# Kernel optimization log

Measured on AMD Instinct MI355X. Metric: run time of the kernel, lower is better.

The kernel has to match this reference:

```python
import jax, jax.numpy as jnp
import numpy as np

DIM = 192
HEADS = 6
HEAD_DIM = DIM // HEADS
WH, WW = 8, 8
N = WH * WW
SCALE = HEAD_DIM ** -0.5


def relative_position_index(wh, ww):
    ch, cw = np.meshgrid(np.arange(wh), np.arange(ww), indexing='ij')
    coords = np.stack([ch.ravel(), cw.ravel()])            # [2, N]
    rel = coords[:, :, None] - coords[:, None, :]          # [2, N, N]
    rel = rel.transpose(1, 2, 0)
    rel[:, :, 0] += wh - 1
    rel[:, :, 1] += ww - 1
    rel[:, :, 0] *= 2 * ww - 1
    return jnp.asarray(rel.sum(-1))                        # [N, N] int


REL_IDX = relative_position_index(WH, WW)


def setup_inputs() -> dict:
    key = jax.random.key(0)
    ks = jax.random.split(key, 12)
    B_ = 4096
    nW = 64
    s = DIM ** -0.5
    inp = {
        'lr_up_windows': jax.random.normal(ks[0], (B_, N, DIM), jnp.float32),
        'ref_down_up_windows': jax.random.normal(ks[1], (B_, N, DIM), jnp.float32),
        'ref_windows': jax.random.normal(ks[2], (B_, N, DIM), jnp.float32),
        'mask': jnp.zeros((nW, N, N), jnp.float32),
        'Wq': jax.random.normal(ks[3], (DIM, DIM), jnp.float32) * s,
        'bq': jnp.zeros((DIM,), jnp.float32),
        'Wk': jax.random.normal(ks[4], (DIM, DIM), jnp.float32) * s,
        'bk': jnp.zeros((DIM,), jnp.float32),
        'Wv': jax.random.normal(ks[5], (DIM, DIM), jnp.float32) * s,
        'bv': jnp.zeros((DIM,), jnp.float32),
        'Wp': jax.random.normal(ks[6], (DIM, DIM), jnp.float32) * s,
        'bp': jnp.zeros((DIM,), jnp.float32),
        'bias_table': jax.random.normal(ks[7], ((2 * WH - 1) * (2 * WW - 1), HEADS), jnp.float32) * 0.02,
    }
    return inp


def reference(lr_up_windows, ref_down_up_windows, ref_windows, mask,
              Wq, bq, Wk, bk, Wv, bv, Wp, bp, bias_table):
    B_, n, C = lr_up_windows.shape
    # projections ([in, out] weights; x @ W + b)
    q = (lr_up_windows @ Wq + bq).reshape(B_, n, HEADS, HEAD_DIM).transpose(0, 2, 1, 3)
    k = (ref_down_up_windows @ Wk + bk).reshape(B_, n, HEADS, HEAD_DIM).transpose(0, 2, 1, 3)
    v = (ref_windows @ Wv + bv).reshape(B_, n, HEADS, HEAD_DIM).transpose(0, 2, 1, 3)
    attn = jnp.einsum('bhnd,bhmd->bhnm', q * SCALE, k)     # [B_, H, N, N]
    rpb = bias_table[REL_IDX]                               # [N, N, H]
    attn = attn + rpb.transpose(2, 0, 1)[None]
    nW = mask.shape[0]
    attn = attn.reshape(B_ // nW, nW, HEADS, n, n) + mask[None, :, None]
    attn = attn.reshape(B_, HEADS, n, n)
    attn = jax.nn.softmax(attn, axis=-1)
    x = jnp.einsum('bhnm,bhmd->bhnd', attn, v).transpose(0, 2, 1, 3).reshape(B_, n, C)
    return x @ Wp + bp
```

## Files before the change

### kernel.cpp

```cpp
#include <hip/hip_runtime.h>
#include <hip/hip_bf16.h>
#include <stdint.h>

typedef short s16x8 __attribute__((ext_vector_type(8)));
typedef short s16x4 __attribute__((ext_vector_type(4)));
typedef float f32x4 __attribute__((ext_vector_type(4)));

#define MFMA16(a, b, c) __builtin_amdgcn_mfma_f32_16x16x32_bf16((a), (b), (c), 0, 0, 0)

__device__ __forceinline__ unsigned short f2bf(float f) {
  union { float f; uint32_t u; } x; x.f = f;
  uint32_t u = x.u;
  return (unsigned short)((u + 0x7FFFu + ((u >> 16) & 1u)) >> 16);
}
__device__ __forceinline__ float bf2f(unsigned short h) {
  union { uint32_t u; float f; } x; x.u = ((uint32_t)h) << 16;
  return x.f;
}
__device__ __forceinline__ void glds16(const void* g, void* l) {
  __builtin_amdgcn_global_load_lds((const __attribute__((address_space(1))) void*)g,
                                   (__attribute__((address_space(3))) void*)l, 16, 0, 0);
}

__global__ __launch_bounds__(256) void prep_weights(
    const float* __restrict__ Wq, const float* __restrict__ Wk,
    const float* __restrict__ Wv, const float* __restrict__ Wp,
    unsigned short* __restrict__ wt) {
  int idx = blockIdx.x * 256 + threadIdx.x;
  if (idx >= 4 * 36864) return;
  int mat = idx / 36864, rem = idx % 36864;
  int n = rem / 192, k = rem % 192;
  const float* W = (mat == 0) ? Wq : (mat == 1) ? Wk : (mat == 2) ? Wv : Wp;
  wt[idx] = f2bf(W[k * 192 + n]);
}

__global__ __launch_bounds__(256) void prep_rpb(
    const float* __restrict__ bias_table, unsigned short* __restrict__ rpb) {
  int idx = blockIdx.x * 256 + threadIdx.x;
  if (idx >= 6 * 4096) return;
  int h = idx / 4096, r = idx % 4096;
  int i = r >> 6, j = r & 63;
  int dh = (i >> 3) - (j >> 3) + 7;
  int dw = (i & 7) - (j & 7) + 7;
  rpb[idx] = f2bf(bias_table[(dh * 15 + dw) * 6 + h]);
}

__global__ __launch_bounds__(256, 3) void pass1_proj(
    const float* __restrict__ X1g, const float* __restrict__ X2g,
    const float* __restrict__ X3g,
    const float* __restrict__ bq, const float* __restrict__ bk,
    const float* __restrict__ bv,
    const unsigned short* __restrict__ wt,
    char* __restrict__ qkv, int B_) {
  extern __shared__ char p1lds[];
  unsigned short* xs = (unsigned short*)p1lds;
  char* ob = p1lds + 25600;
  const int which = blockIdx.x / B_;
  const int w = blockIdx.x - which * B_;
  const int tid = threadIdx.x;
  const int lane = tid & 63;
  const int wv = tid >> 6;
  const int l16 = lane & 15, lq = lane >> 4;
  const float* Xb =
      ((which == 0) ? X1g : (which == 1) ? X2g : X3g) + (size_t)w * 12288;
  const unsigned short* W = wt + which * 36864;
  const int nt0 = wv * 3;

  const float4* Xb4 = (const float4*)Xb;
  float4 xr[12];
#pragma unroll
  for (int r = 0; r < 6; ++r) {
    int p = r * 256 + tid;
    xr[2 * r]     = Xb4[2 * p];
    xr[2 * r + 1] = Xb4[2 * p + 1];
  }

  s16x8 wf[3][6];
#pragma unroll
  for (int t = 0; t < 3; ++t) {
    const unsigned short* wc = W + (size_t)((nt0 + t) * 16 + l16) * 192 + lq * 8;
#pragma unroll
    for (int ks = 0; ks < 6; ++ks) wf[t][ks] = *(const s16x8*)(wc + ks * 32);
  }
  f32x4 bqk[3];
  float bvv[3];
  if (which < 2) {
    const float* bias = which ? bk : bq;
#pragma unroll
    for (int t = 0; t < 3; ++t)
      bqk[t] = *(const f32x4*)&bias[(nt0 + t) * 16 + lq * 4];
  } else {
#pragma unroll
    for (int t = 0; t < 3; ++t) bvv[t] = bv[(nt0 + t) * 16 + l16];
  }

#pragma unroll
  for (int r = 0; r < 6; ++r) {
    int p = r * 256 + tid;
    int row = p / 24, k8 = p - row * 24;
    const float4& a = xr[2 * r];
    const float4& c = xr[2 * r + 1];
    s16x8 t;
    t[0] = (short)f2bf(a.x); t[1] = (short)f2bf(a.y);
    t[2] = (short)f2bf(a.z); t[3] = (short)f2bf(a.w);
    t[4] = (short)f2bf(c.x); t[5] = (short)f2bf(c.y);
    t[6] = (short)f2bf(c.z); t[7] = (short)f2bf(c.w);
    *(s16x8*)&xs[row * 200 + k8 * 8] = t;
  }
  __syncthreads();

  const float scale = (which == 0) ? 0.17677669529663689f : 1.0f;

#pragma unroll
  for (int mi = 0; mi < 4; ++mi) {
    s16x8 xf[6];
    const unsigned short* pr = xs + (mi * 16 + l16) * 200 + lq * 8;
#pragma unroll
    for (int ks = 0; ks < 6; ++ks) xf[ks] = *(const s16x8*)(pr + ks * 32);
    if (which < 2) {
      int tok = mi * 16 + l16;
#pragma unroll
      for (int t = 0; t < 3; ++t) {
        f32x4 acc = bqk[t];
#pragma unroll
        for (int ks = 0; ks < 6; ++ks) acc = MFMA16(wf[t][ks], xf[ks], acc);
        s16x4 pv;
#pragma unroll
        for (int q = 0; q < 4; ++q) pv[q] = (short)f2bf(acc[q] * scale);
        int c = (nt0 + t) * 2 + (lq >> 1);
        *(s16x4*)(ob + tok * 384 + ((c ^ (tok & 7)) << 4) + (lq & 1) * 8) = pv;
      }
    } else {
#pragma unroll
      for (int t = 0; t < 3; ++t) {
        f32x4 acc = {bvv[t], bvv[t], bvv[t], bvv[t]};
#pragma unroll
        for (int ks = 0; ks < 6; ++ks) acc = MFMA16(xf[ks], wf[t][ks], acc);
        int d = (nt0 + t) * 16 + l16;
        int c = (mi >> 1) * 4 + lq;
        s16x4 pv;
#pragma unroll
        for (int q = 0; q < 4; ++q) pv[q] = (short)f2bf(acc[q]);
        *(s16x4*)(ob + d * 128 + ((c ^ (d & 7)) << 4) + (mi & 1) * 8) = pv;
      }
    }
  }
  __syncthreads();

  char* gdst = qkv + (size_t)w * 73728 + which * 24576;
#pragma unroll
  for (int r = 0; r < 6; ++r) {
    int i = (r * 256 + tid) * 16;
    *(float4*)(gdst + i) = *(const float4*)(ob + i);
  }
}

__global__ __launch_bounds__(512, 4) void pass2_attn(
    const char* __restrict__ qkv, const float* __restrict__ maskg,
    const unsigned short* __restrict__ rpb, const float* __restrict__ bp,
    const unsigned short* __restrict__ wt, float* __restrict__ out, int nW) {
  extern __shared__ char lds[];
  const int b = blockIdx.x, tid = threadIdx.x;
  const int wv = tid >> 6, lane = tid & 63;
  const int l16 = lane & 15, lq = lane >> 4;
  const char* Qg = qkv + (size_t)b * 73728;
  const char* KVsrc = Qg + 24576;

#pragma unroll
  for (int r = 0; r < 6; ++r)
    glds16(KVsrc + (size_t)(r * 512 + tid) * 16, lds + (r * 512 + wv * 64) * 16);

  const int mt = wv & 3, g = wv >> 2;
  const int row0 = mt * 16, qg = row0 + l16;
  s16x8 qf[3];
#pragma unroll
  for (int hh = 0; hh < 3; ++hh) {
    int c = (g * 3 + hh) * 4 + lq;
    qf[hh] = *(const s16x8*)(Qg + qg * 384 + ((c ^ (qg & 7)) << 4));
  }
  const float* mrow = maskg + (size_t)(b % nW) * 4096 + qg * 64;
  f32x4 mv[4];
#pragma unroll
  for (int nt = 0; nt < 4; ++nt) mv[nt] = *(const f32x4*)(mrow + nt * 16 + lq * 4);
  s16x4 rv[3][4];
#pragma unroll
  for (int hh = 0; hh < 3; ++hh)
#pragma unroll
    for (int nt = 0; nt < 4; ++nt)
      rv[hh][nt] = *(const s16x4*)&rpb[(g * 3 + hh) * 4096 + qg * 64 + nt * 16 + lq * 4];
  __syncthreads();

  unsigned short* Osm = (unsigned short*)(lds + 49152);
#pragma unroll
  for (int hh = 0; hh < 3; ++hh) {
    int h = g * 3 + hh;
    f32x4 sv[4];
#pragma unroll
    for (int nt = 0; nt < 4; ++nt) {
      int kr = nt * 16 + l16;
      s16x8 ka = *(const s16x8*)(lds + kr * 384 + (((h * 4 + lq) ^ (kr & 7)) << 4));
      f32x4 z = {0.f, 0.f, 0.f, 0.f};
      sv[nt] = MFMA16(ka, qf[hh], z);
    }
    float lg[4][4];
#pragma unroll
    for (int nt = 0; nt < 4; ++nt)
#pragma unroll
      for (int qr = 0; qr < 4; ++qr)
        lg[nt][qr] = sv[nt][qr] + bf2f((unsigned short)rv[hh][nt][qr]) + mv[nt][qr];
    float mx = lg[0][0];
#pragma unroll
    for (int nt = 0; nt < 4; ++nt)
#pragma unroll
      for (int qr = 0; qr < 4; ++qr) mx = fmaxf(mx, lg[nt][qr]);
    mx = fmaxf(mx, __shfl_xor(mx, 16, 64));
    mx = fmaxf(mx, __shfl_xor(mx, 32, 64));
    float p[4][4], sum = 0.f;
#pragma unroll
    for (int nt = 0; nt < 4; ++nt)
#pragma unroll
      for (int qr = 0; qr < 4; ++qr) {
        p[nt][qr] = __expf(lg[nt][qr] - mx);
        sum += p[nt][qr];
      }
    sum += __shfl_xor(sum, 16, 64);
    sum += __shfl_xor(sum, 32, 64);
    float ri = 1.0f / sum;
    s16x8 pa0, pa1;
#pragma unroll
    for (int r = 0; r < 4; ++r) {
      pa0[r]     = (short)f2bf(p[0][r] * ri);
      pa0[4 + r] = (short)f2bf(p[1][r] * ri);
      pa1[r]     = (short)f2bf(p[2][r] * ri);
      pa1[4 + r] = (short)f2bf(p[3][r] * ri);
    }
    f32x4 o0 = {0.f, 0.f, 0.f, 0.f};
    f32x4 o1 = {0.f, 0.f, 0.f, 0.f};
#pragma unroll
    for (int kt = 0; kt < 2; ++kt) {
      int d0 = h * 32 + l16, d1 = h * 32 + 16 + l16;
      s16x8 vb0 = *(const s16x8*)(lds + 24576 + d0 * 128 +
                                  ((((kt << 2) + lq) ^ (d0 & 7)) << 4));
      s16x8 vb1 = *(const s16x8*)(lds + 24576 + d1 * 128 +
                                  ((((kt << 2) + lq) ^ (d1 & 7)) << 4));
      o0 = MFMA16(kt ? pa1 : pa0, vb0, o0);
      o1 = MFMA16(kt ? pa1 : pa0, vb1, o1);
    }
#pragma unroll
    for (int q = 0; q < 4; ++q) {
      int row = row0 + lq * 4 + q;
      Osm[row * 208 + h * 32 + l16]      = f2bf(o0[q]);
      Osm[row * 208 + h * 32 + 16 + l16] = f2bf(o1[q]);
    }
  }
  __syncthreads();

  {
    const unsigned short* W = wt + 3 * 36864;
    float* obp = out + (size_t)b * 12288;
    const int mh = wv >> 2, nh = wv & 3;
    s16x8 a[2][6];
#pragma unroll
    for (int mi = 0; mi < 2; ++mi)
#pragma unroll
      for (int ks = 0; ks < 6; ++ks)
        a[mi][ks] = *(const s16x8*)&Osm[((mh * 2 + mi) * 16 + l16) * 208 +
                                        ks * 32 + lq * 8];
#pragma unroll
    for (int nt2 = 0; nt2 < 3; ++nt2) {
      int col = (nh * 3 + nt2) * 16 + l16;
      float bsv = bp[col];
      f32x4 acc0 = {bsv, bsv, bsv, bsv};
      f32x4 acc1 = {bsv, bsv, bsv, bsv};
      const unsigned short* wc = W + (size_t)col * 192 + lq * 8;
#pragma unroll
      for (int ks = 0; ks < 6; ++ks) {
        s16x8 bb = *(const s16x8*)(wc + ks * 32);
        acc0 = MFMA16(a[0][ks], bb, acc0);
        acc1 = MFMA16(a[1][ks], bb, acc1);
      }
#pragma unroll
      for (int q = 0; q < 4; ++q) {
        obp[((mh * 2 + 0) * 16 + lq * 4 + q) * 192 + col] = acc0[q];
        obp[((mh * 2 + 1) * 16 + lq * 4 + q) * 192 + col] = acc1[q];
      }
    }
  }
}

#define XPAD 200
#define VPAD 72
#define PPAD 72
#define MPAD 66
struct SmemF {
  unsigned short Xs[2][64][XPAD];
  unsigned short Qs[64][XPAD];
  unsigned short Ks[64][XPAD];
  unsigned short VTs[192][VPAD];
  unsigned short Ps[2][64][PPAD];
  unsigned short Ms[64][MPAD];
};

__global__ __launch_bounds__(512, 2) void win_attn_fused(
    const float* __restrict__ X1g, const float* __restrict__ X2g,
    const float* __restrict__ X3g, const float* __restrict__ maskg,
    const float* __restrict__ bq, const float* __restrict__ bk,
    const float* __restrict__ bv, const float* __restrict__ bp,
    const unsigned short* __restrict__ wt, const unsigned short* __restrict__ rpb,
    float* __restrict__ out, int nW) {
  extern __shared__ char smem_raw[];
  SmemF& S = *reinterpret_cast<SmemF*>(smem_raw);
  const int b = blockIdx.x;
  const int tid = threadIdx.x;
  const int wave = tid >> 6, lane = tid & 63;
  const int l16 = lane & 15, lq = lane >> 4;
  const int mh = wave >> 2, nh = wave & 3;

  const float4* x1v = (const float4*)(X1g + (size_t)b * 12288);
  const float4* x2v = (const float4*)(X2g + (size_t)b * 12288);
  const float4* x3v = (const float4*)(X3g + (size_t)b * 12288);
  float4 x3r[6];
#pragma unroll
  for (int it = 0; it < 6; ++it) {
    int i = it * 512 + tid;
    float4 v1 = x1v[i];
    float4 v2 = x2v[i];
    x3r[it] = x3v[i];
    int row = i / 48, c = (i % 48) * 4;
    s16x4 p1, p2;
    p1[0] = (short)f2bf(v1.x); p1[1] = (short)f2bf(v1.y);
    p1[2] = (short)f2bf(v1.z); p1[3] = (short)f2bf(v1.w);
    p2[0] = (short)f2bf(v2.x); p2[1] = (short)f2bf(v2.y);
    p2[2] = (short)f2bf(v2.z); p2[3] = (short)f2bf(v2.w);
    *(s16x4*)&S.Xs[0][row][c] = p1;
    *(s16x4*)&S.Xs[1][row][c] = p2;
  }
  const float* mw = maskg + (size_t)(b % nW) * 4096;
  for (int i = tid; i < 4096; i += 512)
    S.Ms[i >> 6][i & 63] = f2bf(mw[i]);
  __syncthreads();

  auto proj = [&](const unsigned short (*Xsrc)[XPAD], const unsigned short* W,
                  const float* bias, unsigned short (*dst)[XPAD], float scale) {
    s16x8 a[2][6];
#pragma unroll
    for (int mi = 0; mi < 2; ++mi)
#pragma unroll
      for (int ks = 0; ks < 6; ++ks)
        a[mi][ks] = *(const s16x8*)&Xsrc[(mh * 2 + mi) * 16 + l16][ks * 32 + lq * 8];
#pragma unroll
    for (int nt2 = 0; nt2 < 3; ++nt2) {
      int col = (nh * 3 + nt2) * 16 + l16;
      float bsv = bias[col];
      f32x4 acc0 = {bsv, bsv, bsv, bsv};
      f32x4 acc1 = {bsv, bsv, bsv, bsv};
#pragma unroll
      for (int ks = 0; ks < 6; ++ks) {
        s16x8 bb = *(const s16x8*)&W[(size_t)col * 192 + ks * 32 + lq * 8];
        acc0 = MFMA16(a[0][ks], bb, acc0);
        acc1 = MFMA16(a[1][ks], bb, acc1);
      }
#pragma unroll
      for (int q = 0; q < 4; ++q) {
        dst[(mh * 2 + 0) * 16 + lq * 4 + q][col] = f2bf(acc0[q] * scale);
        dst[(mh * 2 + 1) * 16 + lq * 4 + q][col] = f2bf(acc1[q] * scale);
      }
    }
  };

  proj(S.Xs[0], wt + 0 * 36864, bq, S.Qs, 0.17677669529663689f);
  proj(S.Xs[1], wt + 1 * 36864, bk, S.Ks, 1.0f);
  __syncthreads();

#pragma unroll
  for (int it = 0; it < 6; ++it) {
    int i = it * 512 + tid;
    int row = i / 48, c = (i % 48) * 4;
    s16x4 p3;
    p3[0] = (short)f2bf(x3r[it].x); p3[1] = (short)f2bf(x3r[it].y);
    p3[2] = (short)f2bf(x3r[it].z); p3[3] = (short)f2bf(x3r[it].w);
    *(s16x4*)&S.Xs[0][row][c] = p3;
  }
  __syncthreads();

  {
    const unsigned short* W = wt + 2 * 36864;
    s16x8 a[2][6];
#pragma unroll
    for (int mi = 0; mi < 2; ++mi)
#pragma unroll
      for (int ks = 0; ks < 6; ++ks)
        a[mi][ks] = *(const s16x8*)&S.Xs[0][(mh * 2 + mi) * 16 + l16][ks * 32 + lq * 8];
#pragma unroll
    for (int nt2 = 0; nt2 < 3; ++nt2) {
      int col = (nh * 3 + nt2) * 16 + l16;
      float bsv = bv[col];
      f32x4 acc0 = {bsv, bsv, bsv, bsv};
      f32x4 acc1 = {bsv, bsv, bsv, bsv};
#pragma unroll
      for (int ks = 0; ks < 6; ++ks) {
        s16x8 bb = *(const s16x8*)&W[(size_t)col * 192 + ks * 32 + lq * 8];
        acc0 = MFMA16(a[0][ks], bb, acc0);
        acc1 = MFMA16(a[1][ks], bb, acc1);
      }
      s16x4 pv0, pv1;
#pragma unroll
      for (int q = 0; q < 4; ++q) { pv0[q] = (short)f2bf(acc0[q]); pv1[q] = (short)f2bf(acc1[q]); }
      *(s16x4*)&S.VTs[col][(mh * 2 + 0) * 16 + lq * 4] = pv0;
      *(s16x4*)&S.VTs[col][(mh * 2 + 1) * 16 + lq * 4] = pv1;
    }
  }
  __syncthreads();

  {
    const int mt = wave & 3, g = wave >> 2;
    const int row0 = mt * 16;
#pragma unroll 1
    for (int hh = 0; hh < 3; ++hh) {
      int h = g * 3 + hh;
      s16x8 qa = *(const s16x8*)&S.Qs[row0 + l16][h * 32 + lq * 8];
      f32x4 sv[4];
#pragma unroll
      for (int nt = 0; nt < 4; ++nt) {
        s16x8 kb = *(const s16x8*)&S.Ks[nt * 16 + l16][h * 32 + lq * 8];
        f32x4 z = {0.f, 0.f, 0.f, 0.f};
        sv[nt] = MFMA16(qa, kb, z);
      }
      const unsigned short* rpbh = rpb + h * 4096;
      float lg[4][4];
#pragma unroll
      for (int nt = 0; nt < 4; ++nt) {
        int j = nt * 16 + l16;
#pragma unroll
        for (int q = 0; q < 4; ++q) {
          int i = row0 + lq * 4 + q;
          lg[nt][q] = sv[nt][q] + bf2f(rpbh[i * 64 + j]) + bf2f(S.Ms[i][j]);
        }
      }
#pragma unroll
      for (int q = 0; q < 4; ++q) {
        float m = fmaxf(fmaxf(lg[0][q], lg[1][q]), fmaxf(lg[2][q], lg[3][q]));
#pragma unroll
        for (int s = 1; s < 16; s <<= 1) m = fmaxf(m, __shfl_xor(m, s, 64));
        float p[4], sum = 0.f;
#pragma unroll
        for (int nt = 0; nt < 4; ++nt) { p[nt] = __expf(lg[nt][q] - m); sum += p[nt]; }
#pragma unroll
        for (int s = 1; s < 16; s <<= 1) sum += __shfl_xor(sum, s, 64);
        float r = 1.0f / sum;
#pragma unroll
        for (int nt = 0; nt < 4; ++nt)
          S.Ps[g][row0 + lq * 4 + q][nt * 16 + l16] = f2bf(p[nt] * r);
      }
      f32x4 oacc[2] = {{0.f, 0.f, 0.f, 0.f}, {0.f, 0.f, 0.f, 0.f}};
#pragma unroll
      for (int kt = 0; kt < 2; ++kt) {
        s16x8 pa = *(const s16x8*)&S.Ps[g][row0 + l16][kt * 32 + lq * 8];
#pragma unroll
        for (int n2 = 0; n2 < 2; ++n2) {
          s16x8 vb = *(const s16x8*)&S.VTs[h * 32 + n2 * 16 + l16][kt * 32 + lq * 8];
          oacc[n2] = MFMA16(pa, vb, oacc[n2]);
        }
      }
#pragma unroll
      for (int n2 = 0; n2 < 2; ++n2)
#pragma unroll
        for (int q = 0; q < 4; ++q)
          S.Xs[1][row0 + lq * 4 + q][h * 32 + n2 * 16 + l16] = f2bf(oacc[n2][q]);
    }
  }
  __syncthreads();

  {
    const unsigned short* W = wt + 3 * 36864;
    float* ob = out + (size_t)b * 12288;
    s16x8 a[2][6];
#pragma unroll
    for (int mi = 0; mi < 2; ++mi)
#pragma unroll
      for (int ks = 0; ks < 6; ++ks)
        a[mi][ks] = *(const s16x8*)&S.Xs[1][(mh * 2 + mi) * 16 + l16][ks * 32 + lq * 8];
#pragma unroll
    for (int nt2 = 0; nt2 < 3; ++nt2) {
      int col = (nh * 3 + nt2) * 16 + l16;
      float bsv = bp[col];
      f32x4 acc0 = {bsv, bsv, bsv, bsv};
      f32x4 acc1 = {bsv, bsv, bsv, bsv};
#pragma unroll
      for (int ks = 0; ks < 6; ++ks) {
        s16x8 bb = *(const s16x8*)&W[(size_t)col * 192 + ks * 32 + lq * 8];
        acc0 = MFMA16(a[0][ks], bb, acc0);
        acc1 = MFMA16(a[1][ks], bb, acc1);
      }
#pragma unroll
      for (int q = 0; q < 4; ++q) {
        ob[((mh * 2 + 0) * 16 + lq * 4 + q) * 192 + col] = acc0[q];
        ob[((mh * 2 + 1) * 16 + lq * 4 + q) * 192 + col] = acc1[q];
      }
    }
  }
}

extern "C" void kernel_launch(void* const* d_in, const int* in_sizes, int n_in,
                              void* d_out, int out_size, void* d_ws, size_t ws_size,
                              hipStream_t stream) {
  const float* X1 = (const float*)d_in[0];
  const float* X2 = (const float*)d_in[1];
  const float* X3 = (const float*)d_in[2];
  const float* mask = (const float*)d_in[3];
  const float* Wq = (const float*)d_in[4];
  const float* bq = (const float*)d_in[5];
  const float* Wk = (const float*)d_in[6];
  const float* bk = (const float*)d_in[7];
  const float* Wv = (const float*)d_in[8];
  const float* bv = (const float*)d_in[9];
  const float* Wp = (const float*)d_in[10];
  const float* bp = (const float*)d_in[11];
  const float* bt = (const float*)d_in[12];

  unsigned short* wt = (unsigned short*)d_ws;
  unsigned short* rpb = wt + 4 * 36864;

  int B_ = in_sizes[0] / 12288;
  int nW = in_sizes[3] / 4096;

  prep_weights<<<576, 256, 0, stream>>>(Wq, Wk, Wv, Wp, wt);
  prep_rpb<<<96, 256, 0, stream>>>(bt, rpb);

  const size_t qkv_off = 344064;
  const size_t need = qkv_off + (size_t)B_ * 73728;

  if (ws_size >= need) {
    char* qkv = (char*)d_ws + qkv_off;
    (void)hipFuncSetAttribute((const void*)pass1_proj,
                              hipFuncAttributeMaxDynamicSharedMemorySize, 50176);
    pass1_proj<<<3 * B_, 256, 50176, stream>>>(X1, X2, X3, bq, bk, bv, wt, qkv, B_);
    (void)hipFuncSetAttribute((const void*)pass2_attn,
                              hipFuncAttributeMaxDynamicSharedMemorySize, 75776);
    pass2_attn<<<B_, 512, 75776, stream>>>(qkv, mask, rpb, bp, wt,
                                           (float*)d_out, nW);
  } else {
    (void)hipFuncSetAttribute((const void*)win_attn_fused,
                              hipFuncAttributeMaxDynamicSharedMemorySize,
                              (int)sizeof(SmemF));
    win_attn_fused<<<B_, 512, sizeof(SmemF), stream>>>(
        X1, X2, X3, mask, bq, bk, bv, bp, wt, rpb, (float*)d_out, nW);
  }
}
```

Before: 374.3 us.

## Double-buffer pass1 input tiles and raise occupancy to four blocks per CU

The projection kernel now loads and converts its 64x192 input in four 16-row slices into two alternating LDS buffers. The next slice's global load is issued before the current slice's MFMAs, and its bf16 conversion and store happen after them. This shrinks LDS from 50176 to 37376 bytes and cuts the staged input registers from 12 float4 to 3. That lets launch bounds ask for 4 blocks per CU instead of 3, so memory latency can hide better. The cost is an extra __syncthreads per slice.

```diff
diff --git a/kernel.cpp b/kernel.cpp
--- a/kernel.cpp
+++ b/kernel.cpp
@@ -45,7 +45,7 @@
   rpb[idx] = f2bf(bias_table[(dh * 15 + dw) * 6 + h]);
 }
 
-__global__ __launch_bounds__(256, 3) void pass1_proj(
+__global__ __launch_bounds__(256, 4) void pass1_proj(
     const float* __restrict__ X1g, const float* __restrict__ X2g,
     const float* __restrict__ X3g,
     const float* __restrict__ bq, const float* __restrict__ bk,
@@ -54,7 +54,7 @@
     char* __restrict__ qkv, int B_) {
   extern __shared__ char p1lds[];
   unsigned short* xs = (unsigned short*)p1lds;
-  char* ob = p1lds + 25600;
+  char* ob = p1lds + 12800;
   const int which = blockIdx.x / B_;
   const int w = blockIdx.x - which * B_;
   const int tid = threadIdx.x;
@@ -63,17 +63,9 @@
   const int l16 = lane & 15, lq = lane >> 4;
   const float* Xb =
       ((which == 0) ? X1g : (which == 1) ? X2g : X3g) + (size_t)w * 12288;
+  const float4* Xb4 = (const float4*)Xb;
   const unsigned short* W = wt + which * 36864;
   const int nt0 = wv * 3;
-
-  const float4* Xb4 = (const float4*)Xb;
-  float4 xr[12];
-#pragma unroll
-  for (int r = 0; r < 6; ++r) {
-    int p = r * 256 + tid;
-    xr[2 * r]     = Xb4[2 * p];
-    xr[2 * r + 1] = Xb4[2 * p + 1];
-  }
 
   s16x8 wf[3][6];
 #pragma unroll
@@ -94,31 +86,42 @@
     for (int t = 0; t < 3; ++t) bvv[t] = bv[(nt0 + t) * 16 + l16];
   }
 
-#pragma unroll
-  for (int r = 0; r < 6; ++r) {
-    int p = r * 256 + tid;
-    int row = p / 24, k8 = p - row * 24;
-    const float4& a = xr[2 * r];
-    const float4& c = xr[2 * r + 1];
-    s16x8 t;
-    t[0] = (short)f2bf(a.x); t[1] = (short)f2bf(a.y);
-    t[2] = (short)f2bf(a.z); t[3] = (short)f2bf(a.w);
-    t[4] = (short)f2bf(c.x); t[5] = (short)f2bf(c.y);
-    t[6] = (short)f2bf(c.z); t[7] = (short)f2bf(c.w);
-    *(s16x8*)&xs[row * 200 + k8 * 8] = t;
-  }
-  __syncthreads();
-
   const float scale = (which == 0) ? 0.17677669529663689f : 1.0f;
-
-#pragma unroll
-  for (int mi = 0; mi < 4; ++mi) {
+  float4 xr[3];
+
+#define P1_ISSUE(wi)                                        \
+  {                                                         \
+    const float4* src = Xb4 + (wi) * 768;                   \
+    _Pragma("unroll")                                       \
+    for (int j = 0; j < 3; ++j) xr[j] = src[j * 256 + tid]; \
+  }
+#define P1_WRITE(wi)                                          \
+  {                                                           \
+    unsigned short* dst = xs + ((wi) & 1) * 3200;             \
+    _Pragma("unroll")                                         \
+    for (int j = 0; j < 3; ++j) {                             \
+      int p = j * 256 + tid;                                  \
+      int row = p / 48, c = p - row * 48;                     \
+      s16x4 t;                                                \
+      t[0] = (short)f2bf(xr[j].x); t[1] = (short)f2bf(xr[j].y); \
+      t[2] = (short)f2bf(xr[j].z); t[3] = (short)f2bf(xr[j].w); \
+      *(s16x4*)&dst[row * 200 + c * 4] = t;                   \
+    }                                                         \
+  }
+
+  P1_ISSUE(0);
+  P1_WRITE(0);
+  __syncthreads();
+
+#pragma unroll
+  for (int wi = 0; wi < 4; ++wi) {
+    if (wi < 3) P1_ISSUE(wi + 1);
     s16x8 xf[6];
-    const unsigned short* pr = xs + (mi * 16 + l16) * 200 + lq * 8;
+    const unsigned short* pr = xs + (wi & 1) * 3200 + l16 * 200 + lq * 8;
 #pragma unroll
     for (int ks = 0; ks < 6; ++ks) xf[ks] = *(const s16x8*)(pr + ks * 32);
     if (which < 2) {
-      int tok = mi * 16 + l16;
+      int tok = wi * 16 + l16;
 #pragma unroll
       for (int t = 0; t < 3; ++t) {
         f32x4 acc = bqk[t];
@@ -137,15 +140,16 @@
 #pragma unroll
         for (int ks = 0; ks < 6; ++ks) acc = MFMA16(xf[ks], wf[t][ks], acc);
         int d = (nt0 + t) * 16 + l16;
-        int c = (mi >> 1) * 4 + lq;
+        int c = (wi >> 1) * 4 + lq;
         s16x4 pv;
 #pragma unroll
         for (int q = 0; q < 4; ++q) pv[q] = (short)f2bf(acc[q]);
-        *(s16x4*)(ob + d * 128 + ((c ^ (d & 7)) << 4) + (mi & 1) * 8) = pv;
-      }
-    }
-  }
-  __syncthreads();
+        *(s16x4*)(ob + d * 128 + ((c ^ (d & 7)) << 4) + (wi & 1) * 8) = pv;
+      }
+    }
+    if (wi < 3) P1_WRITE(wi + 1);
+    __syncthreads();
+  }
 
   char* gdst = qkv + (size_t)w * 73728 + which * 24576;
 #pragma unroll
@@ -153,6 +157,8 @@
     int i = (r * 256 + tid) * 16;
     *(float4*)(gdst + i) = *(const float4*)(ob + i);
   }
+#undef P1_ISSUE
+#undef P1_WRITE
 }
 
 __global__ __launch_bounds__(512, 4) void pass2_attn(
@@ -533,8 +539,8 @@
   if (ws_size >= need) {
     char* qkv = (char*)d_ws + qkv_off;
     (void)hipFuncSetAttribute((const void*)pass1_proj,
-                              hipFuncAttributeMaxDynamicSharedMemorySize, 50176);
-    pass1_proj<<<3 * B_, 256, 50176, stream>>>(X1, X2, X3, bq, bk, bv, wt, qkv, B_);
+                              hipFuncAttributeMaxDynamicSharedMemorySize, 37376);
+    pass1_proj<<<3 * B_, 256, 37376, stream>>>(X1, X2, X3, bq, bk, bv, wt, qkv, B_);
     (void)hipFuncSetAttribute((const void*)pass2_attn,
                               hipFuncAttributeMaxDynamicSharedMemorySize, 75776);
     pass2_attn<<<B_, 512, 75776, stream>>>(qkv, mask, rpb, bp, wt,
```

Result: slower. 637.7 us (+70.4%).

## Process two windows per projection block with prefetch of the second window

Applied to the files above, without the earlier changes.

The projection kernel now handles two windows per block instead of one, halving the grid. The second window's fp32 input is loaded into registers while the first window's MFMA compute runs, overlapping global loads with compute. The bf16 weight fragments loaded into registers are also reused across both windows. In exchange, register pressure doubles for the input buffers, which may hurt occupancy under launch_bounds(256,3), and there are fewer blocks to spread across the GPU.

```diff
diff --git a/kernel.cpp b/kernel.cpp
--- a/kernel.cpp
+++ b/kernel.cpp
@@ -51,29 +51,47 @@
     const float* __restrict__ bq, const float* __restrict__ bk,
     const float* __restrict__ bv,
     const unsigned short* __restrict__ wt,
-    char* __restrict__ qkv, int B_) {
+    char* __restrict__ qkv, int B_, int Bh) {
   extern __shared__ char p1lds[];
   unsigned short* xs = (unsigned short*)p1lds;
   char* ob = p1lds + 25600;
-  const int which = blockIdx.x / B_;
-  const int w = blockIdx.x - which * B_;
+  const int which = blockIdx.x / Bh;
+  const int wb = blockIdx.x - which * Bh;
+  const int w0 = wb * 2, w1 = w0 + 1;
+  const bool has1 = (w1 < B_);
   const int tid = threadIdx.x;
   const int lane = tid & 63;
   const int wv = tid >> 6;
   const int l16 = lane & 15, lq = lane >> 4;
-  const float* Xb =
-      ((which == 0) ? X1g : (which == 1) ? X2g : X3g) + (size_t)w * 12288;
+  const float* Xg = (which == 0) ? X1g : (which == 1) ? X2g : X3g;
   const unsigned short* W = wt + which * 36864;
   const int nt0 = wv * 3;
-
-  const float4* Xb4 = (const float4*)Xb;
-  float4 xr[12];
-#pragma unroll
-  for (int r = 0; r < 6; ++r) {
-    int p = r * 256 + tid;
-    xr[2 * r]     = Xb4[2 * p];
-    xr[2 * r + 1] = Xb4[2 * p + 1];
-  }
+  const float scale = (which == 0) ? 0.17677669529663689f : 1.0f;
+
+  auto LOADX = [&](int w, float4* xr) {
+    const float4* Xb4 = (const float4*)(Xg + (size_t)w * 12288);
+#pragma unroll
+    for (int r = 0; r < 6; ++r) {
+      int p = r * 256 + tid;
+      xr[2 * r]     = Xb4[2 * p];
+      xr[2 * r + 1] = Xb4[2 * p + 1];
+    }
+  };
+  auto CONVWRITE = [&](const float4* xr) {
+#pragma unroll
+    for (int r = 0; r < 6; ++r) {
+      int p = r * 256 + tid;
+      int row = p / 24, k8 = p - row * 24;
+      const float4& a = xr[2 * r];
+      const float4& c = xr[2 * r + 1];
+      s16x8 t;
+      t[0] = (short)f2bf(a.x); t[1] = (short)f2bf(a.y);
+      t[2] = (short)f2bf(a.z); t[3] = (short)f2bf(a.w);
+      t[4] = (short)f2bf(c.x); t[5] = (short)f2bf(c.y);
+      t[6] = (short)f2bf(c.z); t[7] = (short)f2bf(c.w);
+      *(s16x8*)&xs[row * 200 + k8 * 8] = t;
+    }
+  };
 
   s16x8 wf[3][6];
 #pragma unroll
@@ -94,64 +112,65 @@
     for (int t = 0; t < 3; ++t) bvv[t] = bv[(nt0 + t) * 16 + l16];
   }
 
-#pragma unroll
-  for (int r = 0; r < 6; ++r) {
-    int p = r * 256 + tid;
-    int row = p / 24, k8 = p - row * 24;
-    const float4& a = xr[2 * r];
-    const float4& c = xr[2 * r + 1];
-    s16x8 t;
-    t[0] = (short)f2bf(a.x); t[1] = (short)f2bf(a.y);
-    t[2] = (short)f2bf(a.z); t[3] = (short)f2bf(a.w);
-    t[4] = (short)f2bf(c.x); t[5] = (short)f2bf(c.y);
-    t[6] = (short)f2bf(c.z); t[7] = (short)f2bf(c.w);
-    *(s16x8*)&xs[row * 200 + k8 * 8] = t;
-  }
-  __syncthreads();
-
-  const float scale = (which == 0) ? 0.17677669529663689f : 1.0f;
-
-#pragma unroll
-  for (int mi = 0; mi < 4; ++mi) {
-    s16x8 xf[6];
-    const unsigned short* pr = xs + (mi * 16 + l16) * 200 + lq * 8;
-#pragma unroll
-    for (int ks = 0; ks < 6; ++ks) xf[ks] = *(const s16x8*)(pr + ks * 32);
-    if (which < 2) {
-      int tok = mi * 16 + l16;
-#pragma unroll
-      for (int t = 0; t < 3; ++t) {
-        f32x4 acc = bqk[t];
-#pragma unroll
-        for (int ks = 0; ks < 6; ++ks) acc = MFMA16(wf[t][ks], xf[ks], acc);
-        s16x4 pv;
-#pragma unroll
-        for (int q = 0; q < 4; ++q) pv[q] = (short)f2bf(acc[q] * scale);
-        int c = (nt0 + t) * 2 + (lq >> 1);
-        *(s16x4*)(ob + tok * 384 + ((c ^ (tok & 7)) << 4) + (lq & 1) * 8) = pv;
-      }
-    } else {
-#pragma unroll
-      for (int t = 0; t < 3; ++t) {
-        f32x4 acc = {bvv[t], bvv[t], bvv[t], bvv[t]};
-#pragma unroll
-        for (int ks = 0; ks < 6; ++ks) acc = MFMA16(xf[ks], wf[t][ks], acc);
-        int d = (nt0 + t) * 16 + l16;
-        int c = (mi >> 1) * 4 + lq;
-        s16x4 pv;
-#pragma unroll
-        for (int q = 0; q < 4; ++q) pv[q] = (short)f2bf(acc[q]);
-        *(s16x4*)(ob + d * 128 + ((c ^ (d & 7)) << 4) + (mi & 1) * 8) = pv;
-      }
-    }
-  }
-  __syncthreads();
-
-  char* gdst = qkv + (size_t)w * 73728 + which * 24576;
-#pragma unroll
-  for (int r = 0; r < 6; ++r) {
-    int i = (r * 256 + tid) * 16;
-    *(float4*)(gdst + i) = *(const float4*)(ob + i);
+  auto COMPUTE = [&]() {
+#pragma unroll
+    for (int mi = 0; mi < 4; ++mi) {
+      s16x8 xf[6];
+      const unsigned short* pr = xs + (mi * 16 + l16) * 200 + lq * 8;
+#pragma unroll
+      for (int ks = 0; ks < 6; ++ks) xf[ks] = *(const s16x8*)(pr + ks * 32);
+      if (which < 2) {
+        int tok = mi * 16 + l16;
+#pragma unroll
+        for (int t = 0; t < 3; ++t) {
+          f32x4 acc = bqk[t];
+#pragma unroll
+          for (int ks = 0; ks < 6; ++ks) acc = MFMA16(wf[t][ks], xf[ks], acc);
+          s16x4 pv;
+#pragma unroll
+          for (int q = 0; q < 4; ++q) pv[q] = (short)f2bf(acc[q] * scale);
+          int c = (nt0 + t) * 2 + (lq >> 1);
+          *(s16x4*)(ob + tok * 384 + ((c ^ (tok & 7)) << 4) + (lq & 1) * 8) = pv;
+        }
+      } else {
+#pragma unroll
+        for (int t = 0; t < 3; ++t) {
+          f32x4 acc = {bvv[t], bvv[t], bvv[t], bvv[t]};
+#pragma unroll
+          for (int ks = 0; ks < 6; ++ks) acc = MFMA16(xf[ks], wf[t][ks], acc);
+          int d = (nt0 + t) * 16 + l16;
+          int c = (mi >> 1) * 4 + lq;
+          s16x4 pv;
+#pragma unroll
+          for (int q = 0; q < 4; ++q) pv[q] = (short)f2bf(acc[q]);
+          *(s16x4*)(ob + d * 128 + ((c ^ (d & 7)) << 4) + (mi & 1) * 8) = pv;
+        }
+      }
+    }
+  };
+  auto COPYOUT = [&](int w) {
+    char* gdst = qkv + (size_t)w * 73728 + which * 24576;
+#pragma unroll
+    for (int r = 0; r < 6; ++r) {
+      int i = (r * 256 + tid) * 16;
+      *(float4*)(gdst + i) = *(const float4*)(ob + i);
+    }
+  };
+
+  float4 xrA[12], xrB[12];
+  LOADX(w0, xrA);
+  CONVWRITE(xrA);
+  __syncthreads();
+  if (has1) LOADX(w1, xrB);
+  COMPUTE();
+  __syncthreads();
+  COPYOUT(w0);
+  if (has1) {
+    CONVWRITE(xrB);
+    __syncthreads();
+    COMPUTE();
+    __syncthreads();
+    COPYOUT(w1);
   }
 }
 
@@ -532,9 +551,11 @@
 
   if (ws_size >= need) {
     char* qkv = (char*)d_ws + qkv_off;
+    int Bh = (B_ + 1) / 2;
     (void)hipFuncSetAttribute((const void*)pass1_proj,
                               hipFuncAttributeMaxDynamicSharedMemorySize, 50176);
-    pass1_proj<<<3 * B_, 256, 50176, stream>>>(X1, X2, X3, bq, bk, bv, wt, qkv, B_);
+    pass1_proj<<<3 * Bh, 256, 50176, stream>>>(X1, X2, X3, bq, bk, bv, wt, qkv,
+                                               B_, Bh);
     (void)hipFuncSetAttribute((const void*)pass2_attn,
                               hipFuncAttributeMaxDynamicSharedMemorySize, 75776);
     pass2_attn<<<B_, 512, 75776, stream>>>(qkv, mask, rpb, bp, wt,
```

After: 469.0 us. +25.3%, slower.
